# Kernel tuning notes

Hardware: AMD Instinct MI355X
Metric: run time of the kernel (lower is better)

Reference implementation:

```python
import jax, jax.numpy as jnp
import numpy as np

N_NAMED = 8000   # len(e_dict)
ANON_E = 192     # cfg.anon_e
EMB_DIM = 128    # cfg.emb_dim
N_CLASS = 100
N_REL = 50


def setup_inputs() -> dict:
    key = jax.random.key(0)
    ks = jax.random.split(key, 6)
    s = 1.0 / np.sqrt(EMB_DIM)  # xavier-ish scale
    return {
        "anon_e_emb": jax.random.normal(ks[0], (ANON_E, EMB_DIM), dtype=jnp.float32) * s,
        "e_table": jax.random.normal(ks[1], (N_NAMED, EMB_DIM), dtype=jnp.float32) * s,
        "c_table": jax.random.normal(ks[2], (N_CLASS, EMB_DIM), dtype=jnp.float32) * s,
        "r_table": jax.random.normal(ks[3], (N_REL, EMB_DIM), dtype=jnp.float32) * s,
        "fc0_w": jax.random.normal(ks[4], (1, 2 * EMB_DIM), dtype=jnp.float32) * s,
        "fc0_b": jnp.zeros((1,), dtype=jnp.float32),
        "c_id": 7,
        "r_id": 3,
    }


def reference(anon_e_emb, e_table, c_table, r_table, fc0_w, fc0_b, c_id, r_id):
    """FALCON forward for axiom ObjectSomeValuesFrom(<r> <c>), product t-norm.

    Faithful to _get_c_fs, _get_r_fs, _logical_exist:
      c_fs[j]   = sigmoid(fc_0([c_emb ; e_j]))
      r_fs[i,j] = sigmoid(fc_0([e_i + r_emb ; e_j]))
      out[i]    = max_j r_fs[i,j] * c_fs[j]
    fc_0(cat([l, r])) = l @ w_l + r @ w_r + b  (Linear(2d -> 1)), so the
    [N, N, 2d] concat collapses to two [N] GEMVs plus a broadcast add.
    """
    d = e_table.shape[1]
    e_all = jnp.concatenate([e_table, anon_e_emb], axis=0)  # [N, d]
    w_l = fc0_w[0, :d]   # weights for the left (concat) half
    w_r = fc0_w[0, d:]   # weights for the right half
    b = fc0_b[0]

    c_emb = c_table[c_id]  # [d]
    r_emb = r_table[r_id]  # [d]

    # c_fs: fuzzy membership of every entity in class c  -> [N]
    c_fs = jax.nn.sigmoid(jnp.dot(c_emb, w_l) + e_all @ w_r + b)

    # r_fs[i, j] = sigmoid((e_i + r) . w_l + e_j . w_r + b)  -> [N, N]
    row = (e_all + r_emb) @ w_l  # [N]
    col = e_all @ w_r            # [N]
    r_fs = jax.nn.sigmoid(row[:, None] + col[None, :] + b)

    # _logical_exist with product t-norm: max_j (r_fs * c_fs)
    return jnp.max(r_fs * c_fs[None, :], axis=-1)  # [N]
```

## Files before the change

kernel.cpp:

```cpp
#include <hip/hip_runtime.h>


#define N_NAMED 8000
#define N_ALL   8192
#define D       128
#define K1_BLOCKS (N_ALL / 8)

__global__ __launch_bounds__(256) void k_dots(
    const float* __restrict__ anon_e, const float* __restrict__ e_table,
    const float* __restrict__ fc0_w, float* __restrict__ rowdot,
    float* __restrict__ colmax_part)
{
    const int tid = threadIdx.x;
    const int g   = tid >> 5;
    const int l   = tid & 31;
    const int row = blockIdx.x * 8 + g;

    const float4* rp = (row < N_NAMED)
        ? (const float4*)(e_table + (size_t)row * D)
        : (const float4*)(anon_e + (size_t)(row - N_NAMED) * D);

    float4 e  = rp[l];
    float4 wl = ((const float4*)fc0_w)[l];
    float4 wr = ((const float4*)fc0_w)[32 + l];

    float dl = e.x*wl.x + e.y*wl.y + e.z*wl.z + e.w*wl.w;
    float dr = e.x*wr.x + e.y*wr.y + e.z*wr.z + e.w*wr.w;

    #pragma unroll
    for (int off = 16; off >= 1; off >>= 1) {
        dl += __shfl_xor(dl, off, 64);
        dr += __shfl_xor(dr, off, 64);
    }

    __shared__ float scol[8];
    if (l == 0) { rowdot[row] = dl; scol[g] = dr; }
    __syncthreads();
    if (tid == 0) {
        float m = scol[0];
        #pragma unroll
        for (int i = 1; i < 8; i++) m = fmaxf(m, scol[i]);
        colmax_part[blockIdx.x] = m;
    }
}

__global__ __launch_bounds__(256) void k_final(
    const float* __restrict__ c_table, const float* __restrict__ r_table,
    const float* __restrict__ fc0_w, const float* __restrict__ fc0_b,
    const int* __restrict__ c_id, const int* __restrict__ r_id,
    const float* __restrict__ colmax_part, float* __restrict__ out)
{
    const int tid = threadIdx.x;
    const int i   = blockIdx.x * 256 + tid;

    float m = colmax_part[tid];
    m = fmaxf(m, colmax_part[tid + 256]);
    m = fmaxf(m, colmax_part[tid + 512]);
    m = fmaxf(m, colmax_part[tid + 768]);
    #pragma unroll
    for (int off = 32; off >= 1; off >>= 1)
        m = fmaxf(m, __shfl_xor(m, off, 64));

    __shared__ float swm[4];
    __shared__ float smax;
    if ((tid & 63) == 0) swm[tid >> 6] = m;
    __syncthreads();
    if (tid == 0)
        smax = fmaxf(fmaxf(swm[0], swm[1]), fmaxf(swm[2], swm[3]));
    __syncthreads();
    const float colmax = smax;

    const float b = fc0_b[0];
    const float* cp = c_table + (size_t)c_id[0] * D;
    const float* rp = r_table + (size_t)r_id[0] * D;
    float cw = 0.f, rw = 0.f;
    #pragma unroll 8
    for (int t = 0; t < D; t++) {
        float w = fc0_w[t];
        cw = fmaf(cp[t], w, cw);
        rw = fmaf(rp[t], w, rw);
    }

    float a1 = out[i] + rw + colmax + b;
    float a2 = cw + colmax + b;
    float s1 = 1.f / (1.f + __expf(-a1));
    float s2 = 1.f / (1.f + __expf(-a2));
    out[i] = s1 * s2;
}

extern "C" void kernel_launch(void* const* d_in, const int* in_sizes, int n_in,
                              void* d_out, int out_size, void* d_ws, size_t ws_size,
                              hipStream_t stream) {
    const float* anon_e  = (const float*)d_in[0];
    const float* e_table = (const float*)d_in[1];
    const float* c_table = (const float*)d_in[2];
    const float* r_table = (const float*)d_in[3];
    const float* fc0_w   = (const float*)d_in[4];
    const float* fc0_b   = (const float*)d_in[5];
    const int*   c_id    = (const int*)d_in[6];
    const int*   r_id    = (const int*)d_in[7];
    float* out = (float*)d_out;
    float* ws  = (float*)d_ws;

    k_dots<<<K1_BLOCKS, 256, 0, stream>>>(anon_e, e_table, fc0_w, out, ws);
    k_final<<<N_ALL / 256, 256, 0, stream>>>(c_table, r_table, fc0_w, fc0_b,
                                             c_id, r_id, ws, out);
}
```

Measured before the change: 76.12 us.

## Fuse dot and finalize kernels into one cooperative kernel with grid sync

Merges the two kernels into a single cooperative launch. Each block computes its row and column dots, publishes its partial column max, and then waits on a grid-wide sync before reducing the global max and writing the output. The row dot stays in registers instead of going through global memory, and the second launch is removed. In exchange it needs all 1024 blocks to be co-resident and adds a grid barrier, which may cost more than the launch gap it replaces.

```diff
diff --git a/kernel.cpp b/kernel.cpp
--- a/kernel.cpp
+++ b/kernel.cpp
@@ -1,15 +1,20 @@
 #include <hip/hip_runtime.h>
+#include <hip/hip_cooperative_groups.h>
+
+namespace cg = cooperative_groups;
 
 
 #define N_NAMED 8000
 #define N_ALL   8192
 #define D       128
-#define K1_BLOCKS (N_ALL / 8)
+#define BLOCKS  (N_ALL / 8)
 
-__global__ __launch_bounds__(256) void k_dots(
+__global__ __launch_bounds__(256) void k_fused(
     const float* __restrict__ anon_e, const float* __restrict__ e_table,
-    const float* __restrict__ fc0_w, float* __restrict__ rowdot,
-    float* __restrict__ colmax_part)
+    const float* __restrict__ c_table, const float* __restrict__ r_table,
+    const float* __restrict__ fc0_w, const float* __restrict__ fc0_b,
+    const int* __restrict__ c_id, const int* __restrict__ r_id,
+    float* __restrict__ out, float* __restrict__ colmax_part)
 {
     const int tid = threadIdx.x;
     const int g   = tid >> 5;
@@ -34,7 +39,7 @@
     }
 
     __shared__ float scol[8];
-    if (l == 0) { rowdot[row] = dl; scol[g] = dr; }
+    if (l == 0) scol[g] = dr;
     __syncthreads();
     if (tid == 0) {
         float m = scol[0];
@@ -42,21 +47,22 @@
         for (int i = 1; i < 8; i++) m = fmaxf(m, scol[i]);
         colmax_part[blockIdx.x] = m;
     }
-}
 
-__global__ __launch_bounds__(256) void k_final(
-    const float* __restrict__ c_table, const float* __restrict__ r_table,
-    const float* __restrict__ fc0_w, const float* __restrict__ fc0_b,
-    const int* __restrict__ c_id, const int* __restrict__ r_id,
-    const float* __restrict__ colmax_part, float* __restrict__ out)
-{
-    const int tid = threadIdx.x;
-    const int i   = blockIdx.x * 256 + tid;
+    const float b = fc0_b[0];
+    const float* cp = c_table + (size_t)c_id[0] * D;
+    const float* rr = r_table + (size_t)r_id[0] * D;
+    float cw = 0.f, rw = 0.f;
+    #pragma unroll 8
+    for (int t = 0; t < D; t++) {
+        float w = fc0_w[t];
+        cw = fmaf(cp[t], w, cw);
+        rw = fmaf(rr[t], w, rw);
+    }
 
-    float m = colmax_part[tid];
-    m = fmaxf(m, colmax_part[tid + 256]);
-    m = fmaxf(m, colmax_part[tid + 512]);
-    m = fmaxf(m, colmax_part[tid + 768]);
+    cg::this_grid().sync();
+
+    float m = fmaxf(fmaxf(colmax_part[tid],       colmax_part[tid + 256]),
+                    fmaxf(colmax_part[tid + 512], colmax_part[tid + 768]));
     #pragma unroll
     for (int off = 32; off >= 1; off >>= 1)
         m = fmaxf(m, __shfl_xor(m, off, 64));
@@ -70,22 +76,13 @@
     __syncthreads();
     const float colmax = smax;
 
-    const float b = fc0_b[0];
-    const float* cp = c_table + (size_t)c_id[0] * D;
-    const float* rp = r_table + (size_t)r_id[0] * D;
-    float cw = 0.f, rw = 0.f;
-    #pragma unroll 8
-    for (int t = 0; t < D; t++) {
-        float w = fc0_w[t];
-        cw = fmaf(cp[t], w, cw);
-        rw = fmaf(rp[t], w, rw);
+    if (l == 0) {
+        float a1 = dl + rw + colmax + b;
+        float a2 = cw + colmax + b;
+        float s1 = 1.f / (1.f + __expf(-a1));
+        float s2 = 1.f / (1.f + __expf(-a2));
+        out[row] = s1 * s2;
     }
-
-    float a1 = out[i] + rw + colmax + b;
-    float a2 = cw + colmax + b;
-    float s1 = 1.f / (1.f + __expf(-a1));
-    float s2 = 1.f / (1.f + __expf(-a2));
-    out[i] = s1 * s2;
 }
 
 extern "C" void kernel_launch(void* const* d_in, const int* in_sizes, int n_in,
@@ -102,7 +99,11 @@
     float* out = (float*)d_out;
     float* ws  = (float*)d_ws;
 
-    k_dots<<<K1_BLOCKS, 256, 0, stream>>>(anon_e, e_table, fc0_w, out, ws);
-    k_final<<<N_ALL / 256, 256, 0, stream>>>(c_table, r_table, fc0_w, fc0_b,
-                                             c_id, r_id, ws, out);
+    void* args[] = {
+        (void*)&anon_e, (void*)&e_table, (void*)&c_table, (void*)&r_table,
+        (void*)&fc0_w, (void*)&fc0_b, (void*)&c_id, (void*)&r_id,
+        (void*)&out, (void*)&ws
+    };
+    hipLaunchCooperativeKernel((const void*)k_fused, dim3(BLOCKS), dim3(256),
+                               args, 0, stream);
 }
```

New measurement: 135.2 us. 77.6% more time.
